# Kernel optimization log

Hardware: AMD Instinct MI355X
Metric: run time of the kernel (lower is better)

The kernel has to match this reference:

```python
import jax, jax.numpy as jnp
import numpy as np

DIM = 1024
HEADS = 16
HEAD_DIM = 64
INNER = HEADS * HEAD_DIM


def setup_inputs() -> dict:
    key = jax.random.key(0)
    ks = jax.random.split(key, 6)
    x = jax.random.normal(ks[0], (4, 2048, DIM), dtype=jnp.float32)
    # torch nn.Linear weight shape [out, in]; store as [in, out] for x @ W
    Wq = jax.random.normal(ks[1], (DIM, INNER), dtype=jnp.float32) * (DIM ** -0.5)
    Wk = jax.random.normal(ks[2], (DIM, INNER), dtype=jnp.float32) * (DIM ** -0.5)
    Wv = jax.random.normal(ks[3], (DIM, INNER), dtype=jnp.float32) * (DIM ** -0.5)
    Wo = jax.random.normal(ks[4], (INNER, DIM), dtype=jnp.float32) * (INNER ** -0.5)
    bo = jax.random.normal(ks[5], (DIM,), dtype=jnp.float32) * 0.01
    return {"x": x, "Wq": Wq, "Wk": Wk, "Wv": Wv, "Wo": Wo, "bo": bo}


def reference(x, Wq, Wk, Wv, Wo, bo):
    b, n, _ = x.shape
    # projections, split heads: [b, n, inner] -> [b, h, n, d]
    split = lambda t: t.reshape(b, n, HEADS, HEAD_DIM).transpose(0, 2, 1, 3)
    q = split(x @ Wq)
    k = split(x @ Wk)
    v = split(x @ Wv)
    scale = HEAD_DIM ** -0.5
    sim = jnp.einsum('bhnd,bhmd->bhnm', q, k) * scale
    attn = jax.nn.softmax(sim, axis=-1)
    out = jnp.einsum('bhnm,bhmd->bhnd', attn, v)
    out = out.transpose(0, 2, 1, 3).reshape(b, n, INNER)
    return out @ Wo + bo
```

## Files before the change

kernel.cpp:

```cpp
#include <hip/hip_runtime.h>
#include <hip/hip_bf16.h>
#include <stdint.h>

typedef unsigned short u16;
typedef __bf16 bf16x8_t __attribute__((ext_vector_type(8)));
typedef float f32x4_t __attribute__((ext_vector_type(4)));
typedef float f32x16_t __attribute__((ext_vector_type(16)));
typedef unsigned int u32x2_t __attribute__((ext_vector_type(2)));

__device__ __forceinline__ u16 f2bf(float f) {
    union { float f; uint32_t u; } c; c.f = f;
    uint32_t r = c.u + 0x7FFFu + ((c.u >> 16) & 1u);
    return (u16)(r >> 16);
}

__device__ __forceinline__ uint32_t pk2(float a, float b) {
    union { __bf16 h[2]; uint32_t u; } z;
    z.h[0] = (__bf16)a; z.h[1] = (__bf16)b;
    return z.u;
}

__device__ __forceinline__ void gld_lds16(const void* g, void* l) {
    __builtin_amdgcn_global_load_lds(
        (__attribute__((address_space(1))) void*)(g),
        (__attribute__((address_space(3))) void*)(l), 16, 0, 0);
}

#define QSCALE 0.18033688011112042f

__global__ void k_convert_x(const float* __restrict__ x, u16* __restrict__ xb) {
    int i = blockIdx.x * 256 + threadIdx.x;
    float4 v = ((const float4*)x)[i];
    ushort4 o;
    o.x = f2bf(v.x); o.y = f2bf(v.y); o.z = f2bf(v.z); o.w = f2bf(v.w);
    ((ushort4*)xb)[i] = o;
}

__global__ void k_convert_wT(const float* __restrict__ w0, const float* __restrict__ w1,
                             const float* __restrict__ w2, const float* __restrict__ w3,
                             u16* __restrict__ wT) {
    __shared__ u16 t[32][33];
    const float* src = (blockIdx.z == 0) ? w0 : (blockIdx.z == 1) ? w1 : (blockIdx.z == 2) ? w2 : w3;
    u16* dst = wT + (size_t)blockIdx.z * (1024 * 1024);
    int n0 = blockIdx.x * 32, k0 = blockIdx.y * 32;
    int tx = threadIdx.x & 31, ty = threadIdx.x >> 5;
    #pragma unroll
    for (int r = 0; r < 4; ++r) {
        int kl = ty * 4 + r;
        t[tx][kl] = f2bf(src[(size_t)(k0 + kl) * 1024 + n0 + tx]);
    }
    __syncthreads();
    #pragma unroll
    for (int r = 0; r < 4; ++r) {
        int nl = ty * 4 + r;
        dst[(size_t)(n0 + nl) * 1024 + k0 + tx] = t[nl][tx];
    }
}

template <int MODE>
__global__ __launch_bounds__(256, 2) void k_gemm(
    const u16* __restrict__ A, const u16* __restrict__ WT,
    const float* __restrict__ bias,
    u16* __restrict__ qo, u16* __restrict__ ko, u16* __restrict__ vo,
    float* __restrict__ out) {
    __shared__ u16 lA[128 * 32];
    __shared__ u16 lB[128 * 32];
    const int tid = threadIdx.x, wv = tid >> 6, ln = tid & 63;
    const int lo = ln & 15, jg = ln >> 4;
    const int m0 = blockIdx.x * 128;
    int mat, n0;
    if (MODE == 0) { mat = blockIdx.y >> 3; n0 = (blockIdx.y & 7) * 128; }
    else           { mat = 3;               n0 = blockIdx.y * 128; }
    const u16* Bt = WT + (size_t)mat * (1024 * 1024);
    const int wm = wv >> 1, wn = wv & 1;

    f32x4_t acc[4][4];
    #pragma unroll
    for (int i = 0; i < 4; ++i)
        #pragma unroll
        for (int j = 0; j < 4; ++j) acc[i][j] = (f32x4_t){0.f, 0.f, 0.f, 0.f};

    for (int k0 = 0; k0 < 1024; k0 += 32) {
        __syncthreads();
        #pragma unroll
        for (int is = 0; is < 2; ++is) {
            int c = is * 256 + tid;
            int r = c >> 2;
            int j = (c & 3) ^ ((r >> 1) & 3);
            gld_lds16(A  + (size_t)(m0 + r) * 1024 + k0 + j * 8, &lA[(is * 256 + wv * 64) * 8]);
            gld_lds16(Bt + (size_t)(n0 + r) * 1024 + k0 + j * 8, &lB[(is * 256 + wv * 64) * 8]);
        }
        __syncthreads();
        bf16x8_t af[4], bfr[4];
        #pragma unroll
        for (int i = 0; i < 4; ++i) {
            int r = wm * 64 + i * 16 + lo;
            af[i] = *(const bf16x8_t*)&lA[(r * 4 + (jg ^ ((r >> 1) & 3))) * 8];
        }
        #pragma unroll
        for (int j = 0; j < 4; ++j) {
            int r = wn * 64 + j * 16 + lo;
            bfr[j] = *(const bf16x8_t*)&lB[(r * 4 + (jg ^ ((r >> 1) & 3))) * 8];
        }
        #pragma unroll
        for (int i = 0; i < 4; ++i)
            #pragma unroll
            for (int j = 0; j < 4; ++j)
                acc[i][j] = __builtin_amdgcn_mfma_f32_16x16x32_bf16(af[i], bfr[j], acc[i][j], 0, 0, 0);
    }

    if (MODE == 0) {
        u16* dst = (mat == 0) ? qo : (mat == 1) ? ko : vo;
        float sc = (mat == 0) ? QSCALE : 1.0f;
        #pragma unroll
        for (int j = 0; j < 4; ++j) {
            int col = n0 + wn * 64 + j * 16 + lo;
            int hh = col >> 6, dd = col & 63;
            #pragma unroll
            for (int i = 0; i < 4; ++i)
                #pragma unroll
                for (int rg = 0; rg < 4; ++rg) {
                    int m = m0 + wm * 64 + i * 16 + jg * 4 + rg;
                    int bb = m >> 11, nn = m & 2047;
                    dst[(((size_t)(bb * 16 + hh)) * 2048 + nn) * 64 + dd] = f2bf(acc[i][j][rg] * sc);
                }
        }
    } else {
        #pragma unroll
        for (int j = 0; j < 4; ++j) {
            int col = n0 + wn * 64 + j * 16 + lo;
            float bv = bias[col];
            #pragma unroll
            for (int i = 0; i < 4; ++i)
                #pragma unroll
                for (int rg = 0; rg < 4; ++rg) {
                    int m = m0 + wm * 64 + i * 16 + jg * 4 + rg;
                    out[(size_t)m * 1024 + col] = acc[i][j][rg] + bv;
                }
        }
    }
}

__global__ __launch_bounds__(256, 4) void k_attn(
    const u16* __restrict__ Q, const u16* __restrict__ K,
    const u16* __restrict__ V, u16* __restrict__ ctx) {
    __shared__ __align__(16) u16 Kl[2][64 * 64];
    __shared__ __align__(16) u16 Vt[2][64 * 64];

    const int tid = threadIdx.x, wv = tid >> 6, ln = tid & 63;
    const int lq = ln & 31, hi = ln >> 5;
    const int bh = blockIdx.x;
    const int b = bh >> 4, h = bh & 15;
    const size_t base = (size_t)bh * 2048 * 64;
    const int q0 = blockIdx.y * 128 + wv * 32;

    bf16x8_t bQ[4];
    {
        const u16* qp = Q + base + (size_t)(q0 + lq) * 64 + hi * 8;
        #pragma unroll
        for (int s = 0; s < 4; ++s) bQ[s] = *(const bf16x8_t*)(qp + s * 16);
    }
    bf16x8_t ones;
    #pragma unroll
    for (int e = 0; e < 8; ++e) ones[e] = (__bf16)1.0f;

    f32x16_t acc[2], lacc;
    #pragma unroll
    for (int e = 0; e < 16; ++e) { acc[0][e] = 0.f; acc[1][e] = 0.f; lacc[e] = 0.f; }

    uint4 vreg[2];

    auto stageK = [&](int buf, int kv0) {
        #pragma unroll
        for (int is = 0; is < 2; ++is) {
            int c = is * 256 + tid;
            int r = c >> 3;
            int j = (c & 7) ^ (r & 7);
            gld_lds16(K + base + (size_t)(kv0 + r) * 64 + j * 8,
                      &Kl[buf][(is * 256 + wv * 64) * 8]);
        }
    };
    auto issueV = [&](int kv0) {
        #pragma unroll
        for (int is = 0; is < 2; ++is) {
            int c = is * 256 + tid;
            int kvi = c & 63, d0 = (c >> 6) * 8;
            vreg[is] = *(const uint4*)(V + base + (size_t)(kv0 + kvi) * 64 + d0);
        }
    };
    auto writeV = [&](int buf) {
        #pragma unroll
        for (int is = 0; is < 2; ++is) {
            int c = is * 256 + tid;
            int kvi = c & 63, d0 = (c >> 6) * 8;
            int jk = kvi >> 3, klo = kvi & 7;
            union { uint4 u; u16 s[8]; } vv; vv.u = vreg[is];
            #pragma unroll
            for (int e = 0; e < 8; ++e) {
                int d = d0 + e;
                Vt[buf][d * 64 + ((jk ^ (d & 7)) * 8) + klo] = vv.s[e];
            }
        }
    };

    stageK(0, 0);
    issueV(0);
    writeV(0);
    __syncthreads();

    const int swl = lq & 7;

    for (int t = 0; t < 32; ++t) {
        const int c = t & 1;
        if (t < 31) {
            stageK(c ^ 1, (t + 1) * 64);
            issueV((t + 1) * 64);
        }

        #pragma unroll
        for (int kg = 0; kg < 2; ++kg) {
            f32x16_t z;
            #pragma unroll
            for (int e = 0; e < 16; ++e) z[e] = 0.f;
            __builtin_amdgcn_s_setprio(1);
            #pragma unroll
            for (int s = 0; s < 4; ++s) {
                const bf16x8_t aK = *(const bf16x8_t*)
                    &Kl[c][(kg * 32 + lq) * 64 + (((2 * s + hi) ^ swl) * 8)];
                z = __builtin_amdgcn_mfma_f32_32x32x16_bf16(aK, bQ[s], z, 0, 0, 0);
            }
            __builtin_amdgcn_s_setprio(0);
            uint32_t w[4][2];
            #pragma unroll
            for (int m = 0; m < 4; ++m) {
                float p0 = __builtin_amdgcn_exp2f(z[4 * m + 0]);
                float p1 = __builtin_amdgcn_exp2f(z[4 * m + 1]);
                float p2 = __builtin_amdgcn_exp2f(z[4 * m + 2]);
                float p3 = __builtin_amdgcn_exp2f(z[4 * m + 3]);
                w[m][0] = pk2(p0, p1);
                w[m][1] = pk2(p2, p3);
            }
            __builtin_amdgcn_s_setprio(1);
            #pragma unroll
            for (int sl = 0; sl < 2; ++sl) {
                const int ma = 2 * sl, sp = 2 * kg + sl;
                u32x2_t r0 = __builtin_amdgcn_permlane32_swap(w[ma][0], w[ma + 1][0], false, false);
                u32x2_t r1 = __builtin_amdgcn_permlane32_swap(w[ma][1], w[ma + 1][1], false, false);
                union { uint32_t u[4]; bf16x8_t v; } ap;
                ap.u[0] = r0[0]; ap.u[1] = r1[0]; ap.u[2] = r0[1]; ap.u[3] = r1[1];
                lacc = __builtin_amdgcn_mfma_f32_32x32x16_bf16(ap.v, ones, lacc, 0, 0, 0);
                #pragma unroll
                for (int dh = 0; dh < 2; ++dh) {
                    const bf16x8_t bV = *(const bf16x8_t*)
                        &Vt[c][(dh * 32 + lq) * 64 + (((2 * sp + hi) ^ swl) * 8)];
                    acc[dh] = __builtin_amdgcn_mfma_f32_32x32x16_bf16(ap.v, bV, acc[dh], 0, 0, 0);
                }
            }
            __builtin_amdgcn_s_setprio(0);
        }

        if (t < 31) writeV(c ^ 1);
        __syncthreads();
    }

    f32x16_t linv;
    #pragma unroll
    for (int e = 0; e < 16; ++e) linv[e] = 1.0f / lacc[e];
    #pragma unroll
    for (int dh = 0; dh < 2; ++dh) {
        int d = dh * 32 + lq;
        #pragma unroll
        for (int e = 0; e < 16; ++e) {
            int q = q0 + (e & 3) + 8 * (e >> 2) + 4 * hi;
            ctx[((size_t)(b * 2048 + q)) * 1024 + h * 64 + d] = f2bf(acc[dh][e] * linv[e]);
        }
    }
}

extern "C" void kernel_launch(void* const* d_in, const int* in_sizes, int n_in,
                              void* d_out, int out_size, void* d_ws, size_t ws_size,
                              hipStream_t stream) {
    const float* x  = (const float*)d_in[0];
    const float* Wq = (const float*)d_in[1];
    const float* Wk = (const float*)d_in[2];
    const float* Wv = (const float*)d_in[3];
    const float* Wo = (const float*)d_in[4];
    const float* bo = (const float*)d_in[5];
    float* out = (float*)d_out;

    char* ws = (char*)d_ws;
    u16* xb   = (u16*)(ws);
    u16* wT   = (u16*)(ws + 16777216);
    u16* qb   = (u16*)(ws + 25165824);
    u16* kb   = (u16*)(ws + 41943040);
    u16* vb   = (u16*)(ws + 58720256);
    u16* ctx  = (u16*)(ws + 75497472);

    k_convert_x<<<8192, 256, 0, stream>>>(x, xb);
    k_convert_wT<<<dim3(32, 32, 4), 256, 0, stream>>>(Wq, Wk, Wv, Wo, wT);
    k_gemm<0><<<dim3(64, 24), 256, 0, stream>>>(xb, wT, nullptr, qb, kb, vb, nullptr);
    k_attn<<<dim3(64, 16), 256, 0, stream>>>(qb, kb, vb, ctx);
    k_gemm<1><<<dim3(64, 8), 256, 0, stream>>>(ctx, wT, bo, nullptr, nullptr, nullptr, out);
}
```

Before: 200.8 us.

## Write V pre-transposed from projection GEMM and stage it via async LDS loads

The QKV projection GEMM now stores V in a [b,h,d,n] transposed layout, packing four consecutive tokens per store. The attention kernel can then stage V tiles with direct global-to-LDS loads using the same XOR swizzle as K. This removes the per-iteration register round trip and the scalar transposing LDS writes. The V epilogue becomes vectorized, though its stores now stride across d.

```diff
diff --git a/kernel.cpp b/kernel.cpp
--- a/kernel.cpp
+++ b/kernel.cpp
@@ -61,7 +61,7 @@
 __global__ __launch_bounds__(256, 2) void k_gemm(
     const u16* __restrict__ A, const u16* __restrict__ WT,
     const float* __restrict__ bias,
-    u16* __restrict__ qo, u16* __restrict__ ko, u16* __restrict__ vo,
+    u16* __restrict__ qo, u16* __restrict__ ko, u16* __restrict__ vt,
     float* __restrict__ out) {
     __shared__ u16 lA[128 * 32];
     __shared__ u16 lB[128 * 32];
@@ -110,20 +110,39 @@
     }
 
     if (MODE == 0) {
-        u16* dst = (mat == 0) ? qo : (mat == 1) ? ko : vo;
-        float sc = (mat == 0) ? QSCALE : 1.0f;
-        #pragma unroll
-        for (int j = 0; j < 4; ++j) {
-            int col = n0 + wn * 64 + j * 16 + lo;
-            int hh = col >> 6, dd = col & 63;
-            #pragma unroll
-            for (int i = 0; i < 4; ++i)
+        if (mat == 2) {
+            #pragma unroll
+            for (int j = 0; j < 4; ++j) {
+                int col = n0 + wn * 64 + j * 16 + lo;
+                int hh = col >> 6, dd = col & 63;
                 #pragma unroll
-                for (int rg = 0; rg < 4; ++rg) {
-                    int m = m0 + wm * 64 + i * 16 + jg * 4 + rg;
+                for (int i = 0; i < 4; ++i) {
+                    int m = m0 + wm * 64 + i * 16 + jg * 4;
                     int bb = m >> 11, nn = m & 2047;
-                    dst[(((size_t)(bb * 16 + hh)) * 2048 + nn) * 64 + dd] = f2bf(acc[i][j][rg] * sc);
+                    ushort4 pkv;
+                    pkv.x = f2bf(acc[i][j][0]);
+                    pkv.y = f2bf(acc[i][j][1]);
+                    pkv.z = f2bf(acc[i][j][2]);
+                    pkv.w = f2bf(acc[i][j][3]);
+                    *(ushort4*)&vt[(((size_t)(bb * 16 + hh)) * 64 + dd) * 2048 + nn] = pkv;
                 }
+            }
+        } else {
+            u16* dst = (mat == 0) ? qo : ko;
+            float sc = (mat == 0) ? QSCALE : 1.0f;
+            #pragma unroll
+            for (int j = 0; j < 4; ++j) {
+                int col = n0 + wn * 64 + j * 16 + lo;
+                int hh = col >> 6, dd = col & 63;
+                #pragma unroll
+                for (int i = 0; i < 4; ++i)
+                    #pragma unroll
+                    for (int rg = 0; rg < 4; ++rg) {
+                        int m = m0 + wm * 64 + i * 16 + jg * 4 + rg;
+                        int bb = m >> 11, nn = m & 2047;
+                        dst[(((size_t)(bb * 16 + hh)) * 2048 + nn) * 64 + dd] = f2bf(acc[i][j][rg] * sc);
+                    }
+            }
         }
     } else {
         #pragma unroll
@@ -143,7 +162,7 @@
 
 __global__ __launch_bounds__(256, 4) void k_attn(
     const u16* __restrict__ Q, const u16* __restrict__ K,
-    const u16* __restrict__ V, u16* __restrict__ ctx) {
+    const u16* __restrict__ Vg, u16* __restrict__ ctx) {
     __shared__ __align__(16) u16 Kl[2][64 * 64];
     __shared__ __align__(16) u16 Vt[2][64 * 64];
 
@@ -152,6 +171,7 @@
     const int bh = blockIdx.x;
     const int b = bh >> 4, h = bh & 15;
     const size_t base = (size_t)bh * 2048 * 64;
+    const u16* Vtg = Vg + (size_t)bh * 64 * 2048;
     const int q0 = blockIdx.y * 128 + wv * 32;
 
     bf16x8_t bQ[4];
@@ -167,8 +187,6 @@
     f32x16_t acc[2], lacc;
     #pragma unroll
     for (int e = 0; e < 16; ++e) { acc[0][e] = 0.f; acc[1][e] = 0.f; lacc[e] = 0.f; }
-
-    uint4 vreg[2];
 
     auto stageK = [&](int buf, int kv0) {
         #pragma unroll
@@ -180,32 +198,19 @@
                       &Kl[buf][(is * 256 + wv * 64) * 8]);
         }
     };
-    auto issueV = [&](int kv0) {
+    auto stageV = [&](int buf, int kv0) {
         #pragma unroll
         for (int is = 0; is < 2; ++is) {
             int c = is * 256 + tid;
-            int kvi = c & 63, d0 = (c >> 6) * 8;
-            vreg[is] = *(const uint4*)(V + base + (size_t)(kv0 + kvi) * 64 + d0);
+            int r = c >> 3;
+            int j = (c & 7) ^ (r & 7);
+            gld_lds16(Vtg + (size_t)r * 2048 + kv0 + j * 8,
+                      &Vt[buf][(is * 256 + wv * 64) * 8]);
         }
     };
-    auto writeV = [&](int buf) {
-        #pragma unroll
-        for (int is = 0; is < 2; ++is) {
-            int c = is * 256 + tid;
-            int kvi = c & 63, d0 = (c >> 6) * 8;
-            int jk = kvi >> 3, klo = kvi & 7;
-            union { uint4 u; u16 s[8]; } vv; vv.u = vreg[is];
-            #pragma unroll
-            for (int e = 0; e < 8; ++e) {
-                int d = d0 + e;
-                Vt[buf][d * 64 + ((jk ^ (d & 7)) * 8) + klo] = vv.s[e];
-            }
-        }
-    };
 
     stageK(0, 0);
-    issueV(0);
-    writeV(0);
+    stageV(0, 0);
     __syncthreads();
 
     const int swl = lq & 7;
@@ -214,7 +219,7 @@
         const int c = t & 1;
         if (t < 31) {
             stageK(c ^ 1, (t + 1) * 64);
-            issueV((t + 1) * 64);
+            stageV(c ^ 1, (t + 1) * 64);
         }
 
         #pragma unroll
@@ -259,7 +264,6 @@
             __builtin_amdgcn_s_setprio(0);
         }
 
-        if (t < 31) writeV(c ^ 1);
         __syncthreads();
     }
 
@@ -293,12 +297,12 @@
     u16* wT   = (u16*)(ws + 16777216);
     u16* qb   = (u16*)(ws + 25165824);
     u16* kb   = (u16*)(ws + 41943040);
-    u16* vb   = (u16*)(ws + 58720256);
+    u16* vtb  = (u16*)(ws + 58720256);
     u16* ctx  = (u16*)(ws + 75497472);
 
     k_convert_x<<<8192, 256, 0, stream>>>(x, xb);
     k_convert_wT<<<dim3(32, 32, 4), 256, 0, stream>>>(Wq, Wk, Wv, Wo, wT);
-    k_gemm<0><<<dim3(64, 24), 256, 0, stream>>>(xb, wT, nullptr, qb, kb, vb, nullptr);
-    k_attn<<<dim3(64, 16), 256, 0, stream>>>(qb, kb, vb, ctx);
+    k_gemm<0><<<dim3(64, 24), 256, 0, stream>>>(xb, wT, nullptr, qb, kb, vtb, nullptr);
+    k_attn<<<dim3(64, 16), 256, 0, stream>>>(qb, kb, vtb, ctx);
     k_gemm<1><<<dim3(64, 8), 256, 0, stream>>>(ctx, wT, bo, nullptr, nullptr, nullptr, out);
 }
```

Measured after the change: 195.8 us. 2.5% less time.
